# Performance work log

Measured on AMD Instinct MI355X. Metric: run time of the kernel, lower is better.

The kernel has to match this reference:

```python
import jax, jax.numpy as jnp
import numpy as np
import math

B, H, D = 16384, 50, 128
NU, NI, NQ = 100000, 100000, 1000


def _attn(q, k, v, wq, bq, wk, bk, wv, bv, wo, bo):
    # _AttentionLayer: linear+relu on q/k/v, scaled dot-product attention, linear+relu on output
    q = jax.nn.relu(q @ wq + bq)          # [B,Q,D]
    k = jax.nn.relu(k @ wk + bk)          # [B,K,D]
    v = jax.nn.relu(v @ wv + bv)          # [B,K,D]
    scores = jnp.einsum('bqd,bkd->bqk', q, k) / math.sqrt(D)
    y = jnp.einsum('bqk,bkd->bqd', jax.nn.softmax(scores, axis=-1), v)
    return jax.nn.relu(y @ wo + bo)


def setup_inputs() -> dict:
    key = jax.random.key(0)
    ks = jax.random.split(key, 8)
    s = 1.0 / math.sqrt(D)
    inp = {
        'uids': jax.random.randint(ks[0], (B,), 0, NU),
        'qids': jax.random.randint(ks[1], (B,), 0, NQ),
        'u_movies': jax.random.randint(ks[2], (B, H, 2), 0, NI),
        'user_table': jax.random.normal(ks[3], (NU, D), jnp.float32) * 0.02,
        'query_table': jax.random.normal(ks[4], (NQ, D), jnp.float32) * 0.02,
        'item_table': jax.random.normal(ks[5], (NI, D), jnp.float32) * 0.02,
    }
    for i, n in enumerate(['gat', 'sem']):
        for j, p in enumerate(['q', 'k', 'v', 'o']):
            kk = jax.random.fold_in(key, 100 + i * 4 + j)
            inp[f'{n}_w{p}'] = jax.random.normal(kk, (D, D), jnp.float32) * s
            inp[f'{n}_b{p}'] = jnp.zeros((D,), jnp.float32)
    return inp


def reference(uids, qids, u_movies, user_table, query_table, item_table,
              gat_wq, gat_bq, gat_wk, gat_bk, gat_wv, gat_bv, gat_wo, gat_bo,
              sem_wq, sem_bq, sem_wk, sem_bk, sem_wv, sem_bv, sem_wo, sem_bo):
    node = user_table[uids]                       # [B,D]
    ex_node = query_table[qids]                   # [B,D] (computed but unused downstream, as in source)
    nb = item_table[u_movies[:, :, 0]]            # [B,H,D]
    # GAT over neighbor movies: query = node, keys/values = neighbor item embeddings
    agg = _attn(node[:, None, :], nb, nb,
                gat_wq, gat_bq, gat_wk, gat_bk, gat_wv, gat_bv, gat_wo, gat_bo)[:, 0]  # [B,D]
    _ = node + ex_node  # query_embedding in source (dead code on semantic path)
    keys = jnp.stack([node, agg], axis=1)         # [B,2,D]
    out = _attn(node[:, None, :], keys, keys,
                sem_wq, sem_bq, sem_wk, sem_bk, sem_wv, sem_bv, sem_wo, sem_bo)[:, 0]  # [B,D]
    return out
```

## Files before the change

### kernel.cpp

```cpp
#include <hip/hip_runtime.h>
#include <math.h>

typedef __bf16 bf16_t;
typedef bf16_t bf16x8 __attribute__((ext_vector_type(8)));
typedef float  f32x4  __attribute__((ext_vector_type(4)));
typedef unsigned short u16;

#define B_SZ   16384
#define H_SZ   50
#define NI_SZ  100000
#define SCALE  0.08838834764831845f
#define FRAG_W 32768


struct WPtrs { const float* p[8]; };

__global__ void prep_frags(WPtrs wp, u16* __restrict__ dst)
{
    int tid = blockIdx.x * 256 + threadIdx.x;
    int w = tid >> 14, idx = tid & 16383;
    int k = idx >> 7, n = idx & 127;
    float v = wp.p[w][idx];
    bf16_t hi = (bf16_t)v;
    bf16_t lo = (bf16_t)(v - (float)hi);
    int kk = k >> 5, k32 = k & 31;
    int e  = ((k32 >> 4) & 1) * 4 + (k32 & 3);
    int l4 = (k32 >> 2) & 3;
    int lane = l4 * 16 + (n & 15);
    int pos = ((kk * 8 + (n >> 4)) * 64 + lane) * 8 + e;
    union { bf16_t b; u16 u; } ch, cl; ch.b = hi; cl.b = lo;
    dst[(size_t)w * FRAG_W + pos]         = ch.u;
    dst[(size_t)w * FRAG_W + 16384 + pos] = cl.u;
}

template<int TERMS, bool GATHER, bool OUTBF16, int NWOUT, int NSPLIT>
__global__ __launch_bounds__(256, 4)
void gemmW(const float* __restrict__ A, const int* __restrict__ aidx, int M,
           const u16* __restrict__ frags, int4 widx,
           const float* b0, const float* b1, const float* b2, const float* b3,
           char* o0, char* o1, char* o2, char* o3, int rowStride)
{
    constexpr int SUB  = NWOUT * NSPLIT;
    constexpr int NPER = 8 / NSPLIT;
    __shared__ u16 bounce[OUTBF16 ? 4 * 16 * 136 : 4];
    const int t = threadIdx.x, wave = t >> 6, lane = t & 63;
    const int l15 = lane & 15, l4 = lane >> 4;
    const int totalUnits = (M >> 4) * SUB;

    for (int unit = blockIdx.x * 4 + wave; unit < totalUnits; unit += gridDim.x * 4) {
        const int sub  = unit % SUB;
        const int tile = unit / SUB;
        const int w    = sub / NSPLIT;
        const int half = sub % NSPLIT;
        const int row0 = tile * 16;

        const float* bias = b0; char* out = o0; int wi = widx.x;
        if (NWOUT > 1 && w == 1) { bias = b1; out = o1; wi = widx.y; }
        if (NWOUT > 2 && w == 2) { bias = b2; out = o2; wi = widx.z; }
        if (NWOUT > 3 && w == 3) { bias = b3; out = o3; wi = widx.w; }
        const u16* fh = frags + (size_t)wi * FRAG_W;
        const u16* fl = fh + 16384;

        int arow = row0 + l15;
        long src = GATHER ? (long)aidx[arow] : (long)arow;
        const float* Ar = A + src * 128;
        bf16x8 ahi[4], alo[4];
#pragma unroll
        for (int kk = 0; kk < 4; ++kk) {
            f32x4 a0 = *(const f32x4*)(Ar + kk * 32 + 4 * l4);
            f32x4 a1 = *(const f32x4*)(Ar + kk * 32 + 16 + 4 * l4);
#pragma unroll
            for (int e = 0; e < 4; ++e) {
                bf16_t h0 = (bf16_t)a0[e]; ahi[kk][e] = h0;
                bf16_t h1 = (bf16_t)a1[e]; ahi[kk][4 + e] = h1;
                if (TERMS > 1) {
                    alo[kk][e]     = (bf16_t)(a0[e] - (float)h0);
                    alo[kk][4 + e] = (bf16_t)(a1[e] - (float)h1);
                }
            }
        }

        f32x4 acc[NPER];
#pragma unroll
        for (int ni = 0; ni < NPER; ++ni) acc[ni] = (f32x4){0.f, 0.f, 0.f, 0.f};

#pragma unroll
        for (int kk = 0; kk < 4; ++kk)
#pragma unroll
            for (int ni = 0; ni < NPER; ++ni) {
                int n = half * NPER + ni;
                int foff = ((kk * 8 + n) * 64 + lane) * 8;
                bf16x8 bhi = *(const bf16x8*)(fh + foff);
                acc[ni] = __builtin_amdgcn_mfma_f32_16x16x32_bf16(ahi[kk], bhi, acc[ni], 0, 0, 0);
                if (TERMS > 1)
                    acc[ni] = __builtin_amdgcn_mfma_f32_16x16x32_bf16(alo[kk], bhi, acc[ni], 0, 0, 0);
                if (TERMS > 2) {
                    bf16x8 blo = *(const bf16x8*)(fl + foff);
                    acc[ni] = __builtin_amdgcn_mfma_f32_16x16x32_bf16(ahi[kk], blo, acc[ni], 0, 0, 0);
                }
            }

        if (OUTBF16) {
            u16* bb = (u16*)bounce + wave * (16 * 136);
#pragma unroll
            for (int ni = 0; ni < NPER; ++ni) {
                float bvn = bias[ni * 16 + l15];
#pragma unroll
                for (int r = 0; r < 4; ++r) {
                    float v = acc[ni][r] + bvn;
                    v = v > 0.f ? v : 0.f;
                    union { bf16_t b; u16 u; } c; c.b = (bf16_t)v;
                    bb[(l4 * 4 + r) * 136 + ni * 16 + l15] = c.u;
                }
            }
            __asm__ volatile("s_waitcnt lgkmcnt(0)" ::: "memory");
#pragma unroll
            for (int j = 0; j < 4; ++j) {
                int row = j * 4 + l4;
                const u16* sp = bb + row * 136 + l15 * 8;
                char* ob = out + ((size_t)(row0 + row) * rowStride + l15 * 8) * 2;
                *(ulonglong2*)ob = *(const ulonglong2*)sp;
            }
        } else {
#pragma unroll
            for (int ni = 0; ni < NPER; ++ni) {
                int n = half * NPER + ni;
                float bvn = bias[n * 16 + l15];
#pragma unroll
                for (int r = 0; r < 4; ++r) {
                    float v = acc[ni][r] + bvn;
                    v = v > 0.f ? v : 0.f;
                    *(float*)(out + ((size_t)(row0 + l4 * 4 + r) * rowStride + n * 16 + l15) * 4) = v;
                }
            }
        }
    }
}

__global__ __launch_bounds__(256)
void gat_attn(const float* __restrict__ qg, const u16* __restrict__ kt,
              const u16* __restrict__ vt, const int* __restrict__ um,
              float* __restrict__ y)
{
    __shared__ float qsh[4][128];
    const int wave = threadIdx.x >> 6, lane = threadIdx.x & 63;
    const int b = blockIdx.x * 4 + wave;

    float2 q2 = *(const float2*)(qg + (size_t)b * 128 + lane * 2);
    qsh[wave][lane * 2]     = q2.x;
    qsh[wave][lane * 2 + 1] = q2.y;

    int mrow = (lane < H_SZ) ? um[((size_t)b * H_SZ + lane) * 2] : 0;

    unsigned vreg[H_SZ];
#pragma unroll
    for (int h = 0; h < H_SZ; ++h) {
        int vr = __shfl(mrow, h);
        vreg[h] = *(const unsigned*)(vt + (size_t)vr * 128 + lane * 2);
    }
    __syncthreads();

    float s = -1e30f;
    if (lane < H_SZ) {
        const u16* kr = kt + (size_t)mrow * 128;
        float acc = 0.f;
#pragma unroll
        for (int c = 0; c < 4; ++c) {
            bf16x8 kc[4];
#pragma unroll
            for (int j = 0; j < 4; ++j) kc[j] = *(const bf16x8*)(kr + (c * 4 + j) * 8);
#pragma unroll
            for (int j = 0; j < 4; ++j)
#pragma unroll
                for (int e = 0; e < 8; ++e)
                    acc += (float)kc[j][e] * qsh[wave][(c * 4 + j) * 8 + e];
        }
        s = acc * SCALE;
    }
    float m = s;
#pragma unroll
    for (int off = 32; off; off >>= 1) m = fmaxf(m, __shfl_xor(m, off));
    float p = (lane < H_SZ) ? __expf(s - m) : 0.f;
    float sum = p;
#pragma unroll
    for (int off = 32; off; off >>= 1) sum += __shfl_xor(sum, off);
    p /= sum;

    float ax = 0.f, ay = 0.f;
#pragma unroll
    for (int h = 0; h < H_SZ; ++h) {
        float ph = __shfl(p, h);
        unsigned u = vreg[h];
        ax += ph * __uint_as_float(u << 16);
        ay += ph * __uint_as_float(u & 0xffff0000u);
    }
    *(float2*)(y + (size_t)b * 128 + lane * 2) = (float2){ax, ay};
}

__global__ __launch_bounds__(256)
void sem_attn(const float* __restrict__ qs, const float* __restrict__ k1,
              const float* __restrict__ v1, const float* __restrict__ k2,
              const float* __restrict__ v2, float* __restrict__ out)
{
    const int wave = threadIdx.x >> 6, lane = threadIdx.x & 63;
    const size_t base = ((size_t)(blockIdx.x * 4 + wave)) * 128 + lane * 2;
    float2 q  = *(const float2*)(qs + base);
    float2 a1 = *(const float2*)(k1 + base);
    float2 a2 = *(const float2*)(k2 + base);
    float d1 = q.x * a1.x + q.y * a1.y;
    float d2 = q.x * a2.x + q.y * a2.y;
#pragma unroll
    for (int off = 32; off; off >>= 1) {
        d1 += __shfl_xor(d1, off);
        d2 += __shfl_xor(d2, off);
    }
    float s1 = d1 * SCALE, s2 = d2 * SCALE;
    float m = fmaxf(s1, s2);
    float e1 = __expf(s1 - m), e2 = __expf(s2 - m);
    float inv = 1.f / (e1 + e2);
    float p1 = e1 * inv, p2 = e2 * inv;
    float2 b1 = *(const float2*)(v1 + base);
    float2 b2 = *(const float2*)(v2 + base);
    *(float2*)(out + base) = (float2){p1 * b1.x + p2 * b2.x, p1 * b1.y + p2 * b2.y};
}

extern "C" void kernel_launch(void* const* d_in, const int* in_sizes, int n_in,
                              void* d_out, int out_size, void* d_ws, size_t ws_size,
                              hipStream_t stream)
{
    const int*   uids       = (const int*)d_in[0];
    const int*   um         = (const int*)d_in[2];
    const float* user_table = (const float*)d_in[3];
    const float* item_table = (const float*)d_in[5];
    const float* gwq = (const float*)d_in[6];  const float* gbq = (const float*)d_in[7];
    const float* gwk = (const float*)d_in[8];  const float* gbk = (const float*)d_in[9];
    const float* gwv = (const float*)d_in[10]; const float* gbv = (const float*)d_in[11];
    const float* gwo = (const float*)d_in[12]; const float* gbo = (const float*)d_in[13];
    const float* swq = (const float*)d_in[14]; const float* sbq = (const float*)d_in[15];
    const float* swk = (const float*)d_in[16]; const float* sbk = (const float*)d_in[17];
    const float* swv = (const float*)d_in[18]; const float* sbv = (const float*)d_in[19];
    const float* swo = (const float*)d_in[20]; const float* sbo = (const float*)d_in[21];

    char* ws = (char*)d_ws;
    u16*   kt    = (u16*)ws;   ws += (size_t)NI_SZ * 128 * 2;
    u16*   vt    = (u16*)ws;   ws += (size_t)NI_SZ * 128 * 2;
    u16*   frags = (u16*)ws;   ws += (size_t)8 * FRAG_W * 2;
    float* qg  = (float*)ws;   ws += (size_t)B_SZ * 128 * 4;
    float* qs  = (float*)ws;   ws += (size_t)B_SZ * 128 * 4;
    float* k1  = (float*)ws;   ws += (size_t)B_SZ * 128 * 4;
    float* v1  = (float*)ws;   ws += (size_t)B_SZ * 128 * 4;
    float* yb  = (float*)ws;   ws += (size_t)B_SZ * 128 * 4;
    float* agg = (float*)ws;   ws += (size_t)B_SZ * 128 * 4;
    float* k2 = (float*)kt;
    float* v2 = (float*)vt;
    float* outf = (float*)d_out;

    WPtrs wp; wp.p[0]=gwq; wp.p[1]=gwk; wp.p[2]=gwv; wp.p[3]=gwo;
              wp.p[4]=swq; wp.p[5]=swk; wp.p[6]=swv; wp.p[7]=swo;
    prep_frags<<<512, 256, 0, stream>>>(wp, frags);

    gemmW<1, false, true, 2, 1><<<3125, 256, 0, stream>>>(
        item_table, nullptr, NI_SZ, frags, (int4){1, 2, 0, 0},
        gbk, gbv, nullptr, nullptr,
        (char*)kt, (char*)vt, nullptr, nullptr, 128);

    gemmW<3, true, false, 4, 2><<<2048, 256, 0, stream>>>(
        user_table, uids, B_SZ, frags, (int4){0, 4, 5, 6},
        gbq, sbq, sbk, sbv,
        (char*)qg, (char*)qs, (char*)k1, (char*)v1, 128);

    gat_attn<<<B_SZ / 4, 256, 0, stream>>>(qg, kt, vt, um, yb);

    gemmW<3, false, false, 1, 2><<<512, 256, 0, stream>>>(
        yb, nullptr, B_SZ, frags, (int4){3, 0, 0, 0},
        gbo, nullptr, nullptr, nullptr,
        (char*)agg, nullptr, nullptr, nullptr, 128);

    gemmW<3, false, false, 2, 2><<<1024, 256, 0, stream>>>(
        agg, nullptr, B_SZ, frags, (int4){5, 6, 0, 0},
        sbk, sbv, nullptr, nullptr,
        (char*)k2, (char*)v2, nullptr, nullptr, 128);

    sem_attn<<<B_SZ / 4, 256, 0, stream>>>(qs, k1, v1, k2, v2, agg);

    gemmW<3, false, false, 1, 2><<<512, 256, 0, stream>>>(
        agg, nullptr, B_SZ, frags, (int4){7, 0, 0, 0},
        sbo, nullptr, nullptr, nullptr,
        (char*)outf, nullptr, nullptr, nullptr, 128);
}
```

Measured before the change: 316.8 us.

## Fuse node projections and semantic attention chain into two kernels

```diff
diff --git a/kernel.cpp b/kernel.cpp
--- a/kernel.cpp
+++ b/kernel.cpp
@@ -33,108 +33,217 @@
     dst[(size_t)w * FRAG_W + 16384 + pos] = cl.u;
 }
 
-template<int TERMS, bool GATHER, bool OUTBF16, int NWOUT, int NSPLIT>
+__device__ __forceinline__ void repack8(f32x4 a0, f32x4 a1, bf16x8& hi, bf16x8& lo)
+{
+#pragma unroll
+    for (int e = 0; e < 4; ++e) {
+        bf16_t h0 = (bf16_t)a0[e]; hi[e] = h0; lo[e] = (bf16_t)(a0[e] - (float)h0);
+        bf16_t h1 = (bf16_t)a1[e]; hi[4 + e] = h1; lo[4 + e] = (bf16_t)(a1[e] - (float)h1);
+    }
+}
+
+__device__ __forceinline__ void gemm3(const bf16x8 ahi[4], const bf16x8 alo[4],
+                                      const u16* __restrict__ fh, int lane, f32x4 acc[8])
+{
+#pragma unroll
+    for (int kk = 0; kk < 4; ++kk)
+#pragma unroll
+        for (int n = 0; n < 8; ++n) {
+            int foff = ((kk * 8 + n) * 64 + lane) * 8;
+            bf16x8 bhi = *(const bf16x8*)(fh + foff);
+            bf16x8 blo = *(const bf16x8*)(fh + 16384 + foff);
+            acc[n] = __builtin_amdgcn_mfma_f32_16x16x32_bf16(ahi[kk], bhi, acc[n], 0, 0, 0);
+            acc[n] = __builtin_amdgcn_mfma_f32_16x16x32_bf16(alo[kk], bhi, acc[n], 0, 0, 0);
+            acc[n] = __builtin_amdgcn_mfma_f32_16x16x32_bf16(ahi[kk], blo, acc[n], 0, 0, 0);
+        }
+}
+
+__device__ __forceinline__ void zero8(f32x4 acc[8])
+{
+#pragma unroll
+    for (int n = 0; n < 8; ++n) acc[n] = (f32x4){0.f, 0.f, 0.f, 0.f};
+}
+
+__device__ __forceinline__ void load_afrags(const float* __restrict__ Ar, int l4,
+                                            bf16x8 ahi[4], bf16x8 alo[4])
+{
+#pragma unroll
+    for (int kk = 0; kk < 4; ++kk) {
+        f32x4 a0 = *(const f32x4*)(Ar + kk * 32 + 4 * l4);
+        f32x4 a1 = *(const f32x4*)(Ar + kk * 32 + 16 + 4 * l4);
+        repack8(a0, a1, ahi[kk], alo[kk]);
+    }
+}
+
+__device__ __forceinline__ void store_c(float* __restrict__ dst, const f32x4 acc[8],
+                                        const float* __restrict__ bias,
+                                        int row0, int l15, int l4)
+{
+#pragma unroll
+    for (int n = 0; n < 8; ++n) {
+        float bv = bias[n * 16 + l15];
+#pragma unroll
+        for (int r = 0; r < 4; ++r) {
+            float v = acc[n][r] + bv;
+            v = v > 0.f ? v : 0.f;
+            dst[(size_t)(row0 + l4 * 4 + r) * 128 + n * 16 + l15] = v;
+        }
+    }
+}
+
+__device__ __forceinline__ void lds_c_write(float* __restrict__ Sw, const float vals[8][4],
+                                            int l15, int l4)
+{
+#pragma unroll
+    for (int n = 0; n < 8; ++n)
+#pragma unroll
+        for (int r = 0; r < 4; ++r)
+            Sw[(l4 * 4 + r) * 132 + n * 16 + l15] = vals[n][r];
+}
+
+__device__ __forceinline__ void lds_read_afrags(const float* __restrict__ Sw, int l15, int l4,
+                                                bf16x8 ahi[4], bf16x8 alo[4])
+{
+#pragma unroll
+    for (int kk = 0; kk < 4; ++kk) {
+        f32x4 a0 = *(const f32x4*)(Sw + l15 * 132 + kk * 32 + 4 * l4);
+        f32x4 a1 = *(const f32x4*)(Sw + l15 * 132 + kk * 32 + 16 + 4 * l4);
+        repack8(a0, a1, ahi[kk], alo[kk]);
+    }
+}
+
+#define LGKM_FENCE() do { \
+    __asm__ volatile("s_waitcnt lgkmcnt(0)" ::: "memory"); \
+    __builtin_amdgcn_sched_barrier(0); } while (0)
+
 __global__ __launch_bounds__(256, 4)
-void gemmW(const float* __restrict__ A, const int* __restrict__ aidx, int M,
-           const u16* __restrict__ frags, int4 widx,
-           const float* b0, const float* b1, const float* b2, const float* b3,
-           char* o0, char* o1, char* o2, char* o3, int rowStride)
-{
-    constexpr int SUB  = NWOUT * NSPLIT;
-    constexpr int NPER = 8 / NSPLIT;
-    __shared__ u16 bounce[OUTBF16 ? 4 * 16 * 136 : 4];
+void item_kv(const float* __restrict__ A, const u16* __restrict__ frags,
+             const float* __restrict__ bk, const float* __restrict__ bv,
+             u16* __restrict__ kt, u16* __restrict__ vt)
+{
+    __shared__ u16 bounce[4 * 16 * 136];
     const int t = threadIdx.x, wave = t >> 6, lane = t & 63;
     const int l15 = lane & 15, l4 = lane >> 4;
-    const int totalUnits = (M >> 4) * SUB;
+    const int totalUnits = (NI_SZ >> 4) * 2;
 
     for (int unit = blockIdx.x * 4 + wave; unit < totalUnits; unit += gridDim.x * 4) {
-        const int sub  = unit % SUB;
-        const int tile = unit / SUB;
-        const int w    = sub / NSPLIT;
-        const int half = sub % NSPLIT;
+        const int w = unit & 1, tile = unit >> 1;
         const int row0 = tile * 16;
-
-        const float* bias = b0; char* out = o0; int wi = widx.x;
-        if (NWOUT > 1 && w == 1) { bias = b1; out = o1; wi = widx.y; }
-        if (NWOUT > 2 && w == 2) { bias = b2; out = o2; wi = widx.z; }
-        if (NWOUT > 3 && w == 3) { bias = b3; out = o3; wi = widx.w; }
-        const u16* fh = frags + (size_t)wi * FRAG_W;
-        const u16* fl = fh + 16384;
-
-        int arow = row0 + l15;
-        long src = GATHER ? (long)aidx[arow] : (long)arow;
-        const float* Ar = A + src * 128;
-        bf16x8 ahi[4], alo[4];
+        const float* bias = w ? bv : bk;
+        u16* out = w ? vt : kt;
+        const u16* fh = frags + (size_t)(w ? 2 : 1) * FRAG_W;
+
+        const float* Ar = A + (size_t)(row0 + l15) * 128;
+        bf16x8 ahi[4];
 #pragma unroll
         for (int kk = 0; kk < 4; ++kk) {
             f32x4 a0 = *(const f32x4*)(Ar + kk * 32 + 4 * l4);
             f32x4 a1 = *(const f32x4*)(Ar + kk * 32 + 16 + 4 * l4);
 #pragma unroll
             for (int e = 0; e < 4; ++e) {
-                bf16_t h0 = (bf16_t)a0[e]; ahi[kk][e] = h0;
-                bf16_t h1 = (bf16_t)a1[e]; ahi[kk][4 + e] = h1;
-                if (TERMS > 1) {
-                    alo[kk][e]     = (bf16_t)(a0[e] - (float)h0);
-                    alo[kk][4 + e] = (bf16_t)(a1[e] - (float)h1);
-                }
+                ahi[kk][e]     = (bf16_t)a0[e];
+                ahi[kk][4 + e] = (bf16_t)a1[e];
             }
         }
 
-        f32x4 acc[NPER];
-#pragma unroll
-        for (int ni = 0; ni < NPER; ++ni) acc[ni] = (f32x4){0.f, 0.f, 0.f, 0.f};
-
+        f32x4 acc[8];
+        zero8(acc);
 #pragma unroll
         for (int kk = 0; kk < 4; ++kk)
 #pragma unroll
-            for (int ni = 0; ni < NPER; ++ni) {
-                int n = half * NPER + ni;
+            for (int n = 0; n < 8; ++n) {
                 int foff = ((kk * 8 + n) * 64 + lane) * 8;
                 bf16x8 bhi = *(const bf16x8*)(fh + foff);
-                acc[ni] = __builtin_amdgcn_mfma_f32_16x16x32_bf16(ahi[kk], bhi, acc[ni], 0, 0, 0);
-                if (TERMS > 1)
-                    acc[ni] = __builtin_amdgcn_mfma_f32_16x16x32_bf16(alo[kk], bhi, acc[ni], 0, 0, 0);
-                if (TERMS > 2) {
-                    bf16x8 blo = *(const bf16x8*)(fl + foff);
-                    acc[ni] = __builtin_amdgcn_mfma_f32_16x16x32_bf16(ahi[kk], blo, acc[ni], 0, 0, 0);
-                }
+                acc[n] = __builtin_amdgcn_mfma_f32_16x16x32_bf16(ahi[kk], bhi, acc[n], 0, 0, 0);
             }
 
-        if (OUTBF16) {
-            u16* bb = (u16*)bounce + wave * (16 * 136);
-#pragma unroll
-            for (int ni = 0; ni < NPER; ++ni) {
-                float bvn = bias[ni * 16 + l15];
-#pragma unroll
-                for (int r = 0; r < 4; ++r) {
-                    float v = acc[ni][r] + bvn;
-                    v = v > 0.f ? v : 0.f;
-                    union { bf16_t b; u16 u; } c; c.b = (bf16_t)v;
-                    bb[(l4 * 4 + r) * 136 + ni * 16 + l15] = c.u;
-                }
+        u16* bb = bounce + wave * (16 * 136);
+#pragma unroll
+        for (int n = 0; n < 8; ++n) {
+            float bvn = bias[n * 16 + l15];
+#pragma unroll
+            for (int r = 0; r < 4; ++r) {
+                float v = acc[n][r] + bvn;
+                v = v > 0.f ? v : 0.f;
+                union { bf16_t b; u16 u; } c; c.b = (bf16_t)v;
+                bb[(l4 * 4 + r) * 136 + n * 16 + l15] = c.u;
             }
-            __asm__ volatile("s_waitcnt lgkmcnt(0)" ::: "memory");
-#pragma unroll
-            for (int j = 0; j < 4; ++j) {
-                int row = j * 4 + l4;
-                const u16* sp = bb + row * 136 + l15 * 8;
-                char* ob = out + ((size_t)(row0 + row) * rowStride + l15 * 8) * 2;
-                *(ulonglong2*)ob = *(const ulonglong2*)sp;
-            }
-        } else {
-#pragma unroll
-            for (int ni = 0; ni < NPER; ++ni) {
-                int n = half * NPER + ni;
-                float bvn = bias[n * 16 + l15];
-#pragma unroll
-                for (int r = 0; r < 4; ++r) {
-                    float v = acc[ni][r] + bvn;
-                    v = v > 0.f ? v : 0.f;
-                    *(float*)(out + ((size_t)(row0 + l4 * 4 + r) * rowStride + n * 16 + l15) * 4) = v;
-                }
-            }
-        }
-    }
+        }
+        LGKM_FENCE();
+#pragma unroll
+        for (int j = 0; j < 4; ++j) {
+            int row = j * 4 + l4;
+            const u16* sp = bb + row * 136 + l15 * 8;
+            u16* ob = out + (size_t)(row0 + row) * 128 + l15 * 8;
+            *(ulonglong2*)ob = *(const ulonglong2*)sp;
+        }
+        LGKM_FENCE();
+    }
+}
+
+__global__ __launch_bounds__(256, 1)
+void node4_fused(const float* __restrict__ ut, const int* __restrict__ uids,
+                 const u16* __restrict__ frags,
+                 const float* __restrict__ gbq, const float* __restrict__ sbq,
+                 const float* __restrict__ sbk, const float* __restrict__ sbv,
+                 float* __restrict__ qg, float* __restrict__ qs,
+                 float* __restrict__ v1, float* __restrict__ d1g)
+{
+    const int t = threadIdx.x, wave = t >> 6, lane = t & 63;
+    const int l15 = lane & 15, l4 = lane >> 4;
+    const int tile = blockIdx.x * 4 + wave;
+    const int row0 = tile * 16;
+
+    const float* Ar = ut + (size_t)uids[row0 + l15] * 128;
+    bf16x8 ahi[4], alo[4];
+    load_afrags(Ar, l4, ahi, alo);
+
+    f32x4 acc[8];
+
+    zero8(acc);
+    gemm3(ahi, alo, frags + 0 * FRAG_W, lane, acc);
+    store_c(qg, acc, gbq, row0, l15, l4);
+
+    float qsr[8][4];
+    zero8(acc);
+    gemm3(ahi, alo, frags + 4 * FRAG_W, lane, acc);
+#pragma unroll
+    for (int n = 0; n < 8; ++n) {
+        float bv = sbq[n * 16 + l15];
+#pragma unroll
+        for (int r = 0; r < 4; ++r) {
+            float v = acc[n][r] + bv;
+            qsr[n][r] = v > 0.f ? v : 0.f;
+            qs[(size_t)(row0 + l4 * 4 + r) * 128 + n * 16 + l15] = qsr[n][r];
+        }
+    }
+
+    zero8(acc);
+    gemm3(ahi, alo, frags + 5 * FRAG_W, lane, acc);
+    float d1[4] = {0.f, 0.f, 0.f, 0.f};
+#pragma unroll
+    for (int n = 0; n < 8; ++n) {
+        float bv = sbk[n * 16 + l15];
+#pragma unroll
+        for (int r = 0; r < 4; ++r) {
+            float v = acc[n][r] + bv;
+            v = v > 0.f ? v : 0.f;
+            d1[r] += qsr[n][r] * v;
+        }
+    }
+#pragma unroll
+    for (int r = 0; r < 4; ++r) {
+#pragma unroll
+        for (int off = 8; off; off >>= 1) d1[r] += __shfl_xor(d1[r], off);
+    }
+    if (l15 == 0) {
+#pragma unroll
+        for (int r = 0; r < 4; ++r) d1g[row0 + l4 * 4 + r] = d1[r];
+    }
+
+    zero8(acc);
+    gemm3(ahi, alo, frags + 6 * FRAG_W, lane, acc);
+    store_c(v1, acc, sbv, row0, l15, l4);
 }
 
 __global__ __launch_bounds__(256)
@@ -197,31 +306,105 @@
     *(float2*)(y + (size_t)b * 128 + lane * 2) = (float2){ax, ay};
 }
 
-__global__ __launch_bounds__(256)
-void sem_attn(const float* __restrict__ qs, const float* __restrict__ k1,
-              const float* __restrict__ v1, const float* __restrict__ k2,
-              const float* __restrict__ v2, float* __restrict__ out)
-{
-    const int wave = threadIdx.x >> 6, lane = threadIdx.x & 63;
-    const size_t base = ((size_t)(blockIdx.x * 4 + wave)) * 128 + lane * 2;
-    float2 q  = *(const float2*)(qs + base);
-    float2 a1 = *(const float2*)(k1 + base);
-    float2 a2 = *(const float2*)(k2 + base);
-    float d1 = q.x * a1.x + q.y * a1.y;
-    float d2 = q.x * a2.x + q.y * a2.y;
-#pragma unroll
-    for (int off = 32; off; off >>= 1) {
-        d1 += __shfl_xor(d1, off);
-        d2 += __shfl_xor(d2, off);
-    }
-    float s1 = d1 * SCALE, s2 = d2 * SCALE;
-    float m = fmaxf(s1, s2);
-    float e1 = __expf(s1 - m), e2 = __expf(s2 - m);
-    float inv = 1.f / (e1 + e2);
-    float p1 = e1 * inv, p2 = e2 * inv;
-    float2 b1 = *(const float2*)(v1 + base);
-    float2 b2 = *(const float2*)(v2 + base);
-    *(float2*)(out + base) = (float2){p1 * b1.x + p2 * b2.x, p1 * b1.y + p2 * b2.y};
+__global__ __launch_bounds__(256, 1)
+void sem_fused(const float* __restrict__ yb, const float* __restrict__ qs,
+               const float* __restrict__ v1, const float* __restrict__ d1g,
+               const u16* __restrict__ frags,
+               const float* __restrict__ gbo, const float* __restrict__ sbk,
+               const float* __restrict__ sbv, const float* __restrict__ sbo,
+               float* __restrict__ outf)
+{
+    __shared__ float S[4][16 * 132];
+    const int t = threadIdx.x, wave = t >> 6, lane = t & 63;
+    const int l15 = lane & 15, l4 = lane >> 4;
+    float* Sw = S[wave];
+    const int tile = blockIdx.x * 4 + wave;
+    const int row0 = tile * 16;
+
+    bf16x8 ahi[4], alo[4];
+    load_afrags(yb + (size_t)(row0 + l15) * 128, l4, ahi, alo);
+    f32x4 acc[8];
+    zero8(acc);
+    gemm3(ahi, alo, frags + 3 * FRAG_W, lane, acc);
+
+    float stg[8][4];
+#pragma unroll
+    for (int n = 0; n < 8; ++n) {
+        float bv = gbo[n * 16 + l15];
+#pragma unroll
+        for (int r = 0; r < 4; ++r) {
+            float v = acc[n][r] + bv;
+            stg[n][r] = v > 0.f ? v : 0.f;
+        }
+    }
+    lds_c_write(Sw, stg, l15, l4);
+    LGKM_FENCE();
+    lds_read_afrags(Sw, l15, l4, ahi, alo);
+
+    float k2r[8][4], v2r[8][4];
+    zero8(acc);
+    gemm3(ahi, alo, frags + 5 * FRAG_W, lane, acc);
+#pragma unroll
+    for (int n = 0; n < 8; ++n) {
+        float bv = sbk[n * 16 + l15];
+#pragma unroll
+        for (int r = 0; r < 4; ++r) {
+            float v = acc[n][r] + bv;
+            k2r[n][r] = v > 0.f ? v : 0.f;
+        }
+    }
+    zero8(acc);
+    gemm3(ahi, alo, frags + 6 * FRAG_W, lane, acc);
+#pragma unroll
+    for (int n = 0; n < 8; ++n) {
+        float bv = sbv[n * 16 + l15];
+#pragma unroll
+        for (int r = 0; r < 4; ++r) {
+            float v = acc[n][r] + bv;
+            v2r[n][r] = v > 0.f ? v : 0.f;
+        }
+    }
+
+    float d2[4] = {0.f, 0.f, 0.f, 0.f};
+#pragma unroll
+    for (int n = 0; n < 8; ++n) {
+#pragma unroll
+        for (int r = 0; r < 4; ++r) {
+            float q = qs[(size_t)(row0 + l4 * 4 + r) * 128 + n * 16 + l15];
+            d2[r] += q * k2r[n][r];
+        }
+    }
+#pragma unroll
+    for (int r = 0; r < 4; ++r) {
+#pragma unroll
+        for (int off = 8; off; off >>= 1) d2[r] += __shfl_xor(d2[r], off);
+    }
+    float p1[4], p2[4];
+#pragma unroll
+    for (int r = 0; r < 4; ++r) {
+        float s1 = d1g[row0 + l4 * 4 + r] * SCALE;
+        float s2 = d2[r] * SCALE;
+        float m = fmaxf(s1, s2);
+        float e1 = __expf(s1 - m), e2 = __expf(s2 - m);
+        float inv = 1.f / (e1 + e2);
+        p1[r] = e1 * inv; p2[r] = e2 * inv;
+    }
+#pragma unroll
+    for (int n = 0; n < 8; ++n) {
+#pragma unroll
+        for (int r = 0; r < 4; ++r) {
+            float vv1 = v1[(size_t)(row0 + l4 * 4 + r) * 128 + n * 16 + l15];
+            stg[n][r] = p1[r] * vv1 + p2[r] * v2r[n][r];
+        }
+    }
+
+    LGKM_FENCE();
+    lds_c_write(Sw, stg, l15, l4);
+    LGKM_FENCE();
+    lds_read_afrags(Sw, l15, l4, ahi, alo);
+    zero8(acc);
+    gemm3(ahi, alo, frags + 7 * FRAG_W, lane, acc);
+    store_c(outf, acc, sbo, row0, l15, l4);
 }
 
 extern "C" void kernel_launch(void* const* d_in, const int* in_sizes, int n_in,
@@ -247,44 +430,22 @@
     u16*   frags = (u16*)ws;   ws += (size_t)8 * FRAG_W * 2;
     float* qg  = (float*)ws;   ws += (size_t)B_SZ * 128 * 4;
     float* qs  = (float*)ws;   ws += (size_t)B_SZ * 128 * 4;
-    float* k1  = (float*)ws;   ws += (size_t)B_SZ * 128 * 4;
     float* v1  = (float*)ws;   ws += (size_t)B_SZ * 128 * 4;
     float* yb  = (float*)ws;   ws += (size_t)B_SZ * 128 * 4;
-    float* agg = (float*)ws;   ws += (size_t)B_SZ * 128 * 4;
-    float* k2 = (float*)kt;
-    float* v2 = (float*)vt;
+    float* d1g = (float*)ws;   ws += (size_t)B_SZ * 4;
     float* outf = (float*)d_out;
 
     WPtrs wp; wp.p[0]=gwq; wp.p[1]=gwk; wp.p[2]=gwv; wp.p[3]=gwo;
               wp.p[4]=swq; wp.p[5]=swk; wp.p[6]=swv; wp.p[7]=swo;
     prep_frags<<<512, 256, 0, stream>>>(wp, frags);
 
-    gemmW<1, false, true, 2, 1><<<3125, 256, 0, stream>>>(
-        item_table, nullptr, NI_SZ, frags, (int4){1, 2, 0, 0},
-        gbk, gbv, nullptr, nullptr,
-        (char*)kt, (char*)vt, nullptr, nullptr, 128);
-
-    gemmW<3, true, false, 4, 2><<<2048, 256, 0, stream>>>(
-        user_table, uids, B_SZ, frags, (int4){0, 4, 5, 6},
-        gbq, sbq, sbk, sbv,
-        (char*)qg, (char*)qs, (char*)k1, (char*)v1, 128);
+    item_kv<<<3125, 256, 0, stream>>>(item_table, frags, gbk, gbv, kt, vt);
+
+    node4_fused<<<256, 256, 0, stream>>>(user_table, uids, frags,
+                                         gbq, sbq, sbk, sbv, qg, qs, v1, d1g);
 
     gat_attn<<<B_SZ / 4, 256, 0, stream>>>(qg, kt, vt, um, yb);
 
-    gemmW<3, false, false, 1, 2><<<512, 256, 0, stream>>>(
-        yb, nullptr, B_SZ, frags, (int4){3, 0, 0, 0},
-        gbo, nullptr, nullptr, nullptr,
-        (char*)agg, nullptr, nullptr, nullptr, 128);
-
-    gemmW<3, false, false, 2, 2><<<1024, 256, 0, stream>>>(
-        agg, nullptr, B_SZ, frags, (int4){5, 6, 0, 0},
-        sbk, sbv, nullptr, nullptr,
-        (char*)k2, (char*)v2, nullptr, nullptr, 128);
-
-    sem_attn<<<B_SZ / 4, 256, 0, stream>>>(qs, k1, v1, k2, v2, agg);
-
-    gemmW<3, false, false, 1, 2><<<512, 256, 0, stream>>>(
-        agg, nullptr, B_SZ, frags, (int4){7, 0, 0, 0},
-        sbo, nullptr, nullptr, nullptr,
-        (char*)outf, nullptr, nullptr, nullptr, 128);
-}
+    sem_fused<<<256, 256, 0, stream>>>(yb, qs, v1, d1g, frags,
+                                       gbo, sbk, sbv, sbo, outf);
+}
```

Result: slower. 326.7 us (+3.1%).
